# Kernel tuning notes

Hardware: AMD Instinct MI355X
Metric: run time of the kernel (lower is better)

## Reference

```python
import jax, jax.numpy as jnp
import numpy as np
from jax import lax

B, T_ENC, T_DEC, H, N_INP, OC = 1024, 48, 24, 128, 18, 0
F = N_INP - 1  # encoder1 input features (target column removed)


def _lstm_cell(x, h, c, Wih, Whh, bih, bhh):
    # PyTorch LSTMCell gate order: i, f, g, o
    g = x @ Wih.T + bih + h @ Whh.T + bhh
    i, f, gg, o = jnp.split(g, 4, axis=-1)
    c2 = jax.nn.sigmoid(f) * c + jax.nn.sigmoid(i) * jnp.tanh(gg)
    return jax.nn.sigmoid(o) * jnp.tanh(c2), c2


def setup_inputs() -> dict:
    key = jax.random.key(0)
    ks = jax.random.split(key, 32)
    w = lambda k, s: jax.random.normal(k, s, jnp.float32) * 0.05
    return {
        "input_p_q": jax.random.normal(ks[0], (B, T_ENC, N_INP), jnp.float32),
        "label_p": jax.random.normal(ks[1], (B, T_ENC), jnp.float32),
        "Ue1_W": w(ks[2], (T_ENC, T_ENC)), "Ue1_b": w(ks[3], (T_ENC,)),
        "We1_W": w(ks[4], (T_ENC, 2 * H)),
        "Ve1_W": w(ks[5], (1, T_ENC)), "Ve1_b": w(ks[6], (1,)),
        "Ue2_W": w(ks[7], (T_ENC, T_ENC)), "Ue2_b": w(ks[8], (T_ENC,)),
        "We2_W": w(ks[9], (T_ENC, 2 * H)),
        "Ve2_W": w(ks[10], (1, T_ENC)), "Ve2_b": w(ks[11], (1,)),
        "Ud_W": w(ks[12], (H, H)), "Ud_b": w(ks[13], (H,)),
        "Wd_W": w(ks[14], (H, 2 * H)),
        "Vd_W": w(ks[15], (1, H)), "Vd_b": w(ks[16], (1,)),
        "e1_Wih": w(ks[17], (4 * H, F)), "e1_Whh": w(ks[18], (4 * H, H)),
        "e1_bih": w(ks[19], (4 * H,)), "e1_bhh": w(ks[20], (4 * H,)),
        "e2_Wih": w(ks[21], (4 * H, H + 1)), "e2_Whh": w(ks[22], (4 * H, H)),
        "e2_bih": w(ks[23], (4 * H,)), "e2_bhh": w(ks[24], (4 * H,)),
        "d_Wih": w(ks[25], (4 * H, H)), "d_Whh": w(ks[26], (4 * H, H)),
        "d_bih": w(ks[27], (4 * H,)), "d_bhh": w(ks[28], (4 * H,)),
        "reg_W": w(ks[29], (1, H)), "reg_b": w(ks[30], (1,)),
    }


def reference(input_p_q, label_p, Ue1_W, Ue1_b, We1_W, Ve1_W, Ve1_b,
              Ue2_W, Ue2_b, We2_W, Ve2_W, Ve2_b, Ud_W, Ud_b, Wd_W, Vd_W, Vd_b,
              e1_Wih, e1_Whh, e1_bih, e1_bhh, e2_Wih, e2_Whh, e2_bih, e2_bhh,
              d_Wih, d_Whh, d_bih, d_bhh, reg_W, reg_b):
    b = input_p_q.shape[0]
    # drop the target column OC from the 18 input features
    x = jnp.concatenate([input_p_q[:, :T_ENC, :OC],
                         input_p_q[:, :T_ENC, OC + 1:N_INP]], axis=-1)  # [B,T,F]
    labels = label_p[:, :T_ENC]
    zeros = jnp.zeros((b, H), x.dtype)

    # ---- stage 1: spatial (input) attention + encoder1 LSTM ----
    pre1 = jnp.einsum('btf,st->bfs', x, Ue1_W) + Ue1_b  # Ue1(inputs^T), step-invariant: [B,F,T]

    def step1(carry, x_t):
        h, c = carry
        we = jnp.concatenate([h, c], axis=1) @ We1_W.T            # [B,T]
        e = jnp.tanh(we[:, None, :] + pre1)                        # [B,F,T]
        score = jnp.einsum('bft,t->bf', e, Ve1_W[0]) + Ve1_b[0]    # [B,F]
        h, c = _lstm_cell(x_t * jax.nn.softmax(score, axis=1), h, c,
                          e1_Wih, e1_Whh, e1_bih, e1_bhh)
        return (h, c), h

    _, mid = lax.scan(step1, (zeros, zeros), x.transpose(1, 0, 2))  # [T,B,H]
    mid = jnp.concatenate([mid.transpose(1, 0, 2), labels[:, :, None]], axis=2)  # [B,T,H+1]

    # ---- stage 2: second attention + encoder2 LSTM ----
    pre2 = jnp.einsum('btf,st->bfs', mid, Ue2_W) + Ue2_b  # [B,H+1,T]

    def step2(carry, m_t):
        h, c = carry
        we = jnp.concatenate([h, c], axis=1) @ We2_W.T            # [B,T]
        e = jnp.tanh(we[:, None, :] + pre2)                        # [B,H+1,T]
        score = jnp.einsum('bft,t->bf', e, Ve2_W[0]) + Ve2_b[0]    # [B,H+1]
        h, c = _lstm_cell(m_t * jax.nn.softmax(score, axis=1), h, c,
                          e2_Wih, e2_Whh, e2_bih, e2_bhh)
        return (h, c), h

    _, fin = lax.scan(step2, (zeros, zeros), mid.transpose(1, 0, 2))
    fin = fin.transpose(1, 0, 2)  # final_output: [B,T,H]

    # ---- decoder: temporal attention over final_output ----
    ud = fin @ Ud_W.T + Ud_b  # Ud(final_output), step-invariant: [B,T,H]

    def stepd(carry, _):
        hi, ci = carry
        wd = jnp.concatenate([hi, ci], axis=1) @ Wd_W.T            # [B,H]
        e = jnp.tanh(wd[:, None, :] + ud)                           # [B,T,H]
        score = jnp.einsum('bth,h->bt', e, Vd_W[0]) + Vd_b[0]       # [B,T]
        din = jnp.einsum('bt,bth->bh', jax.nn.softmax(score, axis=1), fin)
        hi, ci = _lstm_cell(din, hi, ci, d_Wih, d_Whh, d_bih, d_bhh)
        return (hi, ci), hi

    _, dec = lax.scan(stepd, (zeros, zeros), None, length=T_DEC + 6)  # [Td+6,B,H]
    out = dec.transpose(1, 0, 2) @ reg_W.T + reg_b                     # [B,Td+6,1]
    return out[:, -T_DEC:, 0]                                          # [B,T_DEC]
```

## Files before the change

### kernel.cpp

```cpp
#include <hip/hip_runtime.h>


#define T_ENC 48
#define H 128
#define FDIM 17
#define BBLK 2
#define NTH 512
#define GRID 512

#define H_WT1   0
#define H_WT2   77824
#define H_WTD   212992
#define H_WE1T  344064
#define H_WE2T  356352
#define H_WDT   368640
#define H_UDT   401408
#define F_B1    208896
#define F_B2    209408
#define F_BD    209920
#define F_MID   210432
#define F_FIN   6551040

typedef _Float16 h2_t __attribute__((ext_vector_type(2)));
union H2U { h2_t h; uint u; float f; };

__device__ __forceinline__ h2_t uh(uint v){ H2U x; x.u = v; return x.h; }
__device__ __forceinline__ h2_t fh(float v){ H2U x; x.f = v; return x.h; }
__device__ __forceinline__ uint pack2(float a, float b){
    H2U x; x.h[0] = (_Float16)a; x.h[1] = (_Float16)b; return x.u;
}
__device__ __forceinline__ float dot2f(h2_t a, h2_t b, float c){
#if __has_builtin(__builtin_amdgcn_fdot2)
    return __builtin_amdgcn_fdot2(a, b, c, false);
#else
    return c + (float)a[0]*(float)b[0] + (float)a[1]*(float)b[1];
#endif
}

__device__ __forceinline__ float fast_sigm(float x){
    return __fdividef(1.0f, 1.0f + __expf(-x));
}
__device__ __forceinline__ float fast_tanh(float x){
    float xc = fminf(fmaxf(x, -9.0f), 9.0f);
    float e = __expf(2.0f * xc);
    return __fdividef(e - 1.0f, e + 1.0f);
}

__global__ void prep_kernel(const float* __restrict__ We1W, const float* __restrict__ We2W,
                            const float* __restrict__ WdW,  const float* __restrict__ UdW,
                            const float* __restrict__ e1Wih, const float* __restrict__ e1Whh,
                            const float* __restrict__ e1bih, const float* __restrict__ e1bhh,
                            const float* __restrict__ e2Wih, const float* __restrict__ e2Whh,
                            const float* __restrict__ e2bih, const float* __restrict__ e2bhh,
                            const float* __restrict__ dWih,  const float* __restrict__ dWhh,
                            const float* __restrict__ dbih,  const float* __restrict__ dbhh,
                            float* __restrict__ ws)
{
    int idx = blockIdx.x * blockDim.x + threadIdx.x;
    _Float16* wsh = (_Float16*)ws;
    if (idx < 77824) {
        int k8 = idx >> 12, r = idx & 4095, j = r >> 3, kq = r & 7, k = k8*8 + kq;
        float v = 0.f;
        if (k < 17) v = e1Wih[j*17 + k]; else if (k < 145) v = e1Whh[j*128 + (k-17)];
        wsh[H_WT1 + idx] = (_Float16)v; return;
    }
    idx -= 77824;
    if (idx < 135168) {
        int k8 = idx >> 12, r = idx & 4095, j = r >> 3, kq = r & 7, k = k8*8 + kq;
        float v = 0.f;
        if (k < 129) v = e2Wih[j*129 + k]; else if (k < 257) v = e2Whh[j*128 + (k-129)];
        wsh[H_WT2 + idx] = (_Float16)v; return;
    }
    idx -= 135168;
    if (idx < 131072) {
        int k8 = idx >> 12, r = idx & 4095, j = r >> 3, kq = r & 7, k = k8*8 + kq;
        float v = (k < 128) ? dWih[j*128 + k] : dWhh[j*128 + (k-128)];
        wsh[H_WTD + idx] = (_Float16)v; return;
    }
    idx -= 131072;
    if (idx < 12288) {
        int pr = idx >> 1, p = idx & 1, k2 = pr / 48, s = pr % 48;
        wsh[H_WE1T + idx] = (_Float16)We1W[s*256 + 2*k2 + p]; return;
    }
    idx -= 12288;
    if (idx < 12288) {
        int pr = idx >> 1, p = idx & 1, k2 = pr / 48, s = pr % 48;
        wsh[H_WE2T + idx] = (_Float16)We2W[s*256 + 2*k2 + p]; return;
    }
    idx -= 12288;
    if (idx < 32768) {
        int pr = idx >> 1, p = idx & 1, k2 = pr >> 7, sp = pr & 127;
        wsh[H_WDT + idx] = (_Float16)WdW[sp*256 + 2*k2 + p]; return;
    }
    idx -= 32768;
    if (idx < 16384) {
        int pr = idx >> 1, p = idx & 1, k2 = pr >> 7, hh = pr & 127;
        wsh[H_UDT + idx] = (_Float16)UdW[hh*128 + 2*k2 + p]; return;
    }
    idx -= 16384;
    if (idx < 512) { ws[F_B1 + idx] = e1bih[idx] + e1bhh[idx]; return; }
    idx -= 512;
    if (idx < 512) { ws[F_B2 + idx] = e2bih[idx] + e2bhh[idx]; return; }
    idx -= 512;
    if (idx < 512) { ws[F_BD + idx] = dbih[idx] + dbhh[idx]; return; }
}

template<int K8>
__device__ __forceinline__ void lstm_gates2h(const float4* __restrict__ W8,
                                             const float* __restrict__ bias,
                                             const uint* u2, float* g, int tid)
{
    float a0 = bias[tid], a1 = a0;
    #pragma unroll 4
    for (int k8 = 0; k8 < K8; ++k8) {
        float4 w  = W8[k8*512 + tid];
        float4 ua = *(const float4*)(u2 + 4*k8);
        float4 ub = *(const float4*)(u2 + 132 + 4*k8);
        a0 = dot2f(fh(w.x), fh(ua.x), a0); a0 = dot2f(fh(w.y), fh(ua.y), a0);
        a0 = dot2f(fh(w.z), fh(ua.z), a0); a0 = dot2f(fh(w.w), fh(ua.w), a0);
        a1 = dot2f(fh(w.x), fh(ub.x), a1); a1 = dot2f(fh(w.y), fh(ub.y), a1);
        a1 = dot2f(fh(w.z), fh(ub.z), a1); a1 = dot2f(fh(w.w), fh(ub.w), a1);
    }
    g[tid] = a0; g[512 + tid] = a1;
}

__device__ __forceinline__ void softmax2(float* sc, float* at, int n, int tid)
{
    if (tid < 64) {
        int b = tid >> 5, i = tid & 31, base = b*129;
        float m = -1e30f;
        for (int f = i; f < n; f += 32) m = fmaxf(m, sc[base + f]);
        for (int o = 16; o; o >>= 1) m = fmaxf(m, __shfl_xor(m, o, 32));
        float ssum = 0.f;
        for (int f = i; f < n; f += 32) { float p = __expf(sc[base+f] - m); at[base+f] = p; ssum += p; }
        for (int o = 16; o; o >>= 1) ssum += __shfl_xor(ssum, o, 32);
        float inv = __fdividef(1.f, ssum);
        for (int f = i; f < n; f += 32) at[base + f] *= inv;
    }
}

__device__ __forceinline__ void we_phase_h(const uint* __restrict__ W2,
                                           const uint* h2, const uint* c2,
                                           float* sh_we, int tid)
{
    if (tid < 384) {
        int b = tid / 192, r = tid % 192, s = r >> 2, kq = r & 3;
        const uint* st2 = ((kq < 2) ? h2 : c2) + b*64 + (kq & 1)*32;
        const uint* w2  = W2 + (kq*32)*48 + s;
        float acc = 0.f;
        #pragma unroll 8
        for (int kk = 0; kk < 32; ++kk)
            acc = dot2f(uh(st2[kk]), uh(w2[kk*48]), acc);
        acc += __shfl_xor(acc, 1);
        acc += __shfl_xor(acc, 2);
        if (kq == 0) sh_we[b*48 + s] = acc;
    }
}

__global__ __launch_bounds__(NTH, 6)
void dstp_main(const float* __restrict__ ipq,  const float* __restrict__ labp,
               const float* __restrict__ Ue1W, const float* __restrict__ Ue1b,
               const float* __restrict__ Ve1,  const float* __restrict__ Ve1b,
               const float* __restrict__ Ue2W, const float* __restrict__ Ue2b,
               const float* __restrict__ Ve2,  const float* __restrict__ Ve2b,
               const float* __restrict__ Udb,
               const float* __restrict__ Vd,   const float* __restrict__ Vdb,
               const float* __restrict__ regW, const float* __restrict__ regb,
               float* __restrict__ ws, float* __restrict__ out)
{
    extern __shared__ float sm[];
    float* sh_h   = sm;
    float* sh_c   = sm + 256;
    float* sh_we  = sm + 512;
    float* sh_sc  = sm + 768;
    float* sh_at  = sm + 1028;
    float* sh_g   = sm + 1288;
    float* sh_x   = sm + 2312;
    float* sh_p1  = sm + 3944;
    uint*  sh_h2u = (uint*)(sm + 5576);
    uint*  sh_c2u = (uint*)(sm + 5704);
    uint*  sh_u2  = (uint*)(sm + 5832);
    _Float16* sh_bigh = (_Float16*)(sm + 6096);

    const int tid = threadIdx.x;
    const int b0  = blockIdx.x * BBLK;
    const _Float16* wsh = (const _Float16*)ws;

    for (int idx = tid; idx < BBLK*T_ENC*FDIM; idx += NTH) {
        int b = idx / (T_ENC*FDIM), r = idx % (T_ENC*FDIM), t = r / FDIM, f = r % FDIM;
        sh_x[idx] = ipq[((size_t)(b0 + b)*T_ENC + t)*18 + 1 + f];
    }
    if (tid < 256) { sh_h[tid] = 0.f; sh_c[tid] = 0.f; }
    if (tid < 128) { sh_h2u[tid] = 0u; sh_c2u[tid] = 0u; }
    if (tid < BBLK*T_ENC) {
        int b = tid / T_ENC, t = tid % T_ENC;
        ws[F_MID + ((size_t)(b0 + b)*T_ENC + t)*129 + 128] = labp[(size_t)(b0 + b)*T_ENC + t];
    }
    __syncthreads();
    for (int idx = tid; idx < BBLK*T_ENC*FDIM; idx += NTH) {
        int b = idx / (T_ENC*FDIM), r = idx % (T_ENC*FDIM), s = r / FDIM, f = r % FDIM;
        float acc = Ue1b[s];
        #pragma unroll 4
        for (int t = 0; t < T_ENC; ++t) acc = fmaf(sh_x[(b*T_ENC+t)*FDIM + f], Ue1W[s*T_ENC + t], acc);
        sh_p1[(b*T_ENC + s)*FDIM + f] = acc;
    }
    __syncthreads();

    const float ve1b = Ve1b[0];
    for (int t = 0; t < T_ENC; ++t) {
        we_phase_h((const uint*)(wsh + H_WE1T), sh_h2u, sh_c2u, sh_we, tid);
        __syncthreads();
        if (tid < 136) {
            int pair = tid >> 2, q = tid & 3, b = pair / FDIM, f = pair % FDIM;
            float acc = 0.f;
            for (int s = q; s < 48; s += 4)
                acc += fast_tanh(sh_we[b*48 + s] + sh_p1[(b*T_ENC + s)*FDIM + f]) * Ve1[s];
            acc += __shfl_xor(acc, 1);
            acc += __shfl_xor(acc, 2);
            if (q == 0) sh_sc[b*129 + f] = acc + ve1b;
        }
        __syncthreads();
        softmax2(sh_sc, sh_at, FDIM, tid);
        __syncthreads();
        if (tid < BBLK*152) {
            int b = tid / 152, kk = tid % 152;
            float v;
            if (kk < FDIM)        v = sh_x[(b*T_ENC + t)*FDIM + kk] * sh_at[b*129 + kk];
            else if (kk < FDIM+H) v = sh_h[b*H + (kk - FDIM)];
            else                  v = 0.f;
            float vnb = __shfl_xor(v, 1);
            if (!(tid & 1)) sh_u2[b*132 + (kk >> 1)] = pack2(v, vnb);
        }
        __syncthreads();
        lstm_gates2h<19>((const float4*)(wsh + H_WT1), ws + F_B1, sh_u2, sh_g, tid);
        __syncthreads();
        if (tid < 256) {
            int b = tid >> 7, jj = tid & 127;
            float gi = sh_g[b*512 + jj],       gf = sh_g[b*512 + 128 + jj];
            float gg = sh_g[b*512 + 256 + jj], go = sh_g[b*512 + 384 + jj];
            float c2v = fast_sigm(gf)*sh_c[tid] + fast_sigm(gi)*fast_tanh(gg);
            float hn  = fast_sigm(go)*fast_tanh(c2v);
            sh_c[tid] = c2v; sh_h[tid] = hn;
            ws[F_MID + ((size_t)(b0 + b)*T_ENC + t)*129 + jj] = hn;
            float hnb = __shfl_xor(hn, 1), cnb = __shfl_xor(c2v, 1);
            if (!(jj & 1)) {
                sh_h2u[b*64 + (jj >> 1)] = pack2(hn, hnb);
                sh_c2u[b*64 + (jj >> 1)] = pack2(c2v, cnb);
            }
        }
        __syncthreads();
    }

    for (int idx = tid; idx < BBLK*48*129; idx += NTH) {
        int b = idx / (48*129), r = idx % (48*129), s = r / 129, f = r % 129;
        const float* midb = ws + F_MID + (size_t)(b0 + b)*T_ENC*129 + f;
        float acc = Ue2b[s];
        #pragma unroll 4
        for (int t2 = 0; t2 < T_ENC; ++t2) acc = fmaf(midb[t2*129], Ue2W[s*48 + t2], acc);
        sh_bigh[(b*48 + s)*130 + f] = (_Float16)acc;
    }
    if (tid < 256) { sh_h[tid] = 0.f; sh_c[tid] = 0.f; }
    if (tid < 128) { sh_h2u[tid] = 0u; sh_c2u[tid] = 0u; }
    __syncthreads();

    const float ve2b = Ve2b[0];
    for (int t = 0; t < T_ENC; ++t) {
        we_phase_h((const uint*)(wsh + H_WE2T), sh_h2u, sh_c2u, sh_we, tid);
        __syncthreads();
        if (tid < 258) {
            int b = tid / 129, f = tid % 129;
            const _Float16* p2 = sh_bigh + b*48*130 + f;
            const float* wv = sh_we + b*48;
            float acc = 0.f;
            #pragma unroll 4
            for (int s = 0; s < 48; ++s)
                acc += fast_tanh(wv[s] + (float)p2[s*130]) * Ve2[s];
            sh_sc[b*129 + f] = acc + ve2b;
        }
        __syncthreads();
        softmax2(sh_sc, sh_at, 129, tid);
        __syncthreads();
        for (int idx = tid; idx < BBLK*264; idx += NTH) {
            int b = idx / 264, kk = idx % 264;
            const float* midrow = ws + F_MID + ((size_t)(b0 + b)*T_ENC + t)*129;
            float v;
            if (kk < 129)      v = midrow[kk] * sh_at[b*129 + kk];
            else if (kk < 257) v = sh_h[b*H + (kk - 129)];
            else               v = 0.f;
            float vnb = __shfl_xor(v, 1);
            if (!(idx & 1)) sh_u2[b*132 + ((kk) >> 1)] = pack2(v, vnb);
        }
        __syncthreads();
        lstm_gates2h<33>((const float4*)(wsh + H_WT2), ws + F_B2, sh_u2, sh_g, tid);
        __syncthreads();
        if (tid < 256) {
            int b = tid >> 7, jj = tid & 127;
            float gi = sh_g[b*512 + jj],       gf = sh_g[b*512 + 128 + jj];
            float gg = sh_g[b*512 + 256 + jj], go = sh_g[b*512 + 384 + jj];
            float c2v = fast_sigm(gf)*sh_c[tid] + fast_sigm(gi)*fast_tanh(gg);
            float hn  = fast_sigm(go)*fast_tanh(c2v);
            sh_c[tid] = c2v; sh_h[tid] = hn;
            ws[F_FIN + ((size_t)(b0 + b)*T_ENC + t)*128 + jj] = hn;
            float hnb = __shfl_xor(hn, 1), cnb = __shfl_xor(c2v, 1);
            if (!(jj & 1)) {
                sh_h2u[b*64 + (jj >> 1)] = pack2(hn, hnb);
                sh_c2u[b*64 + (jj >> 1)] = pack2(c2v, cnb);
            }
        }
        __syncthreads();
    }

    {
        uint* fin2 = (uint*)sh_bigh;
        const float4* fsrc = (const float4*)(ws + F_FIN + (size_t)b0*T_ENC*128);
        for (int idx = tid; idx < BBLK*T_ENC*32; idx += NTH) {
            float4 v = fsrc[idx];
            fin2[2*idx]     = pack2(v.x, v.y);
            fin2[2*idx + 1] = pack2(v.z, v.w);
        }
    }
    __syncthreads();
    {
        const int hh = tid & 127;
        const uint* UT2  = (const uint*)(wsh + H_UDT);
        const uint* fin2 = (const uint*)sh_bigh;
        float* uds = ws + F_MID + (size_t)b0*T_ENC*129;
        #pragma unroll
        for (int c = 0; c < 3; ++c) {
            float acc[8]; int rowb2[8];
            #pragma unroll
            for (int i = 0; i < 8; ++i) {
                int idx = (c*8 + i)*NTH + tid;
                int b = idx / 6144, r = idx % 6144, tt = r >> 7;
                rowb2[i] = (b*T_ENC + tt)*64;
                acc[i] = Udb[hh];
            }
            for (int k2 = 0; k2 < 64; ++k2) {
                h2_t w2 = uh(UT2[k2*128 + hh]);
                #pragma unroll
                for (int i = 0; i < 8; ++i) acc[i] = dot2f(uh(fin2[rowb2[i] + k2]), w2, acc[i]);
            }
            #pragma unroll
            for (int i = 0; i < 8; ++i) uds[(size_t)(c*8 + i)*NTH + tid] = acc[i];
        }
    }
    if (tid < 256) { sh_h[tid] = 0.f; sh_c[tid] = 0.f; }
    if (tid < 128) { sh_h2u[tid] = 0u; sh_c2u[tid] = 0u; }
    __syncthreads();
    {
        const float* uds = ws + F_MID + (size_t)b0*T_ENC*129;
        for (int idx = tid; idx < BBLK*T_ENC*128; idx += NTH) {
            int b = idx / 6144, r = idx % 6144, tt = r >> 7, h2i = r & 127;
            sh_bigh[(b*T_ENC + tt)*130 + h2i] = (_Float16)uds[idx];
        }
    }
    __syncthreads();

    const float vdb = Vdb[0], rb = regb[0];
    const float* fing = ws + F_FIN + (size_t)b0*T_ENC*128;
    for (int st = 0; st < 30; ++st) {
        {
            int b = tid >> 8, r = tid & 255, kh = r >> 7, sp = r & 127;
            const uint* st2 = (kh ? sh_c2u : sh_h2u) + b*64;
            const uint* W2  = (const uint*)(wsh + H_WDT) + (kh*64)*128 + sp;
            float acc = 0.f;
            #pragma unroll 8
            for (int kk = 0; kk < 64; ++kk)
                acc = dot2f(uh(st2[kk]), uh(W2[kk*128]), acc);
            sh_g[(b*2 + kh)*128 + sp] = acc;
        }
        __syncthreads();
        if (tid < 192) {
            int q = tid & 1, pair = tid >> 1, b = pair / 48, tt = pair % 48;
            const float* pg = sh_g + b*256;
            const _Float16* udrow = sh_bigh + (b*T_ENC + tt)*130;
            float acc = 0.f;
            int h0 = q*64;
            #pragma unroll 4
            for (int kk = 0; kk < 64; ++kk) {
                int hh = h0 + kk;
                float wd = pg[hh] + pg[128 + hh];
                acc += fast_tanh(wd + (float)udrow[hh]) * Vd[hh];
            }
            acc += __shfl_xor(acc, 1);
            if (q == 0) sh_sc[b*129 + tt] = acc + vdb;
        }
        __syncthreads();
        softmax2(sh_sc, sh_at, 48, tid);
        __syncthreads();
        if (tid < 256) {
            int b = tid >> 7, hh = tid & 127;
            const float* fb = fing + b*T_ENC*128 + hh;
            float acc = 0.f;
            #pragma unroll 4
            for (int tt = 0; tt < 48; ++tt) acc = fmaf(sh_at[b*129 + tt], fb[tt*128], acc);
            float anb = __shfl_xor(acc, 1);
            if (!(hh & 1)) sh_u2[b*132 + (hh >> 1)] = pack2(acc, anb);
        }
        if (tid < 128) {
            int b = tid >> 6, i = tid & 63;
            sh_u2[b*132 + 64 + i] = sh_h2u[b*64 + i];
        }
        __syncthreads();
        lstm_gates2h<32>((const float4*)(wsh + H_WTD), ws + F_BD, sh_u2, sh_g, tid);
        __syncthreads();
        if (tid < 256) {
            int b = tid >> 7, jj = tid & 127;
            float gi = sh_g[b*512 + jj],       gf = sh_g[b*512 + 128 + jj];
            float gg = sh_g[b*512 + 256 + jj], go = sh_g[b*512 + 384 + jj];
            float c2v = fast_sigm(gf)*sh_c[tid] + fast_sigm(gi)*fast_tanh(gg);
            float hn  = fast_sigm(go)*fast_tanh(c2v);
            sh_c[tid] = c2v; sh_h[tid] = hn;
            float hnb = __shfl_xor(hn, 1), cnb = __shfl_xor(c2v, 1);
            if (!(jj & 1)) {
                sh_h2u[b*64 + (jj >> 1)] = pack2(hn, hnb);
                sh_c2u[b*64 + (jj >> 1)] = pack2(c2v, cnb);
            }
        }
        __syncthreads();
        if (st >= 6 && tid < 128) {
            int b = tid >> 6, l = tid & 63;
            float v = sh_h[b*H + l]*regW[l] + sh_h[b*H + 64 + l]*regW[64 + l];
            for (int o = 32; o; o >>= 1) v += __shfl_xor(v, o);
            if (l == 0) out[(size_t)(b0 + b)*24 + (st - 6)] = v + rb;
        }
    }
}

extern "C" void kernel_launch(void* const* d_in, const int* in_sizes, int n_in,
                              void* d_out, int out_size, void* d_ws, size_t ws_size,
                              hipStream_t stream)
{
    const float* ipq   = (const float*)d_in[0];
    const float* labp  = (const float*)d_in[1];
    const float* Ue1W  = (const float*)d_in[2];
    const float* Ue1b  = (const float*)d_in[3];
    const float* We1W  = (const float*)d_in[4];
    const float* Ve1   = (const float*)d_in[5];
    const float* Ve1b  = (const float*)d_in[6];
    const float* Ue2W  = (const float*)d_in[7];
    const float* Ue2b  = (const float*)d_in[8];
    const float* We2W  = (const float*)d_in[9];
    const float* Ve2   = (const float*)d_in[10];
    const float* Ve2b  = (const float*)d_in[11];
    const float* UdW   = (const float*)d_in[12];
    const float* Udb   = (const float*)d_in[13];
    const float* WdW   = (const float*)d_in[14];
    const float* Vd    = (const float*)d_in[15];
    const float* Vdb   = (const float*)d_in[16];
    const float* e1Wih = (const float*)d_in[17];
    const float* e1Whh = (const float*)d_in[18];
    const float* e1bih = (const float*)d_in[19];
    const float* e1bhh = (const float*)d_in[20];
    const float* e2Wih = (const float*)d_in[21];
    const float* e2Whh = (const float*)d_in[22];
    const float* e2bih = (const float*)d_in[23];
    const float* e2bhh = (const float*)d_in[24];
    const float* dWih  = (const float*)d_in[25];
    const float* dWhh  = (const float*)d_in[26];
    const float* dbih  = (const float*)d_in[27];
    const float* dbhh  = (const float*)d_in[28];
    const float* regW  = (const float*)d_in[29];
    const float* regb  = (const float*)d_in[30];
    float* ws  = (float*)d_ws;
    float* out = (float*)d_out;

    prep_kernel<<<(417792 + 1536 + 255)/256, 256, 0, stream>>>(
        We1W, We2W, WdW, UdW,
        e1Wih, e1Whh, e1bih, e1bhh,
        e2Wih, e2Whh, e2bih, e2bhh,
        dWih, dWhh, dbih, dbhh, ws);

    const size_t smem = 12336u * sizeof(float);
    hipFuncSetAttribute((const void*)dstp_main,
                        hipFuncAttributeMaxDynamicSharedMemorySize, (int)smem);
    dstp_main<<<GRID, NTH, smem, stream>>>(
        ipq, labp, Ue1W, Ue1b, Ve1, Ve1b,
        Ue2W, Ue2b, Ve2, Ve2b,
        Udb, Vd, Vdb, regW, regb, ws, out);
}
```

Measured before the change: 1.814 ms.

## Double block threads, split per-step reductions, keep final_output in LDS as fp16

```diff
diff --git a/kernel.cpp b/kernel.cpp
--- a/kernel.cpp
+++ b/kernel.cpp
@@ -5,7 +5,7 @@
 #define H 128
 #define FDIM 17
 #define BBLK 2
-#define NTH 512
+#define NTH 1024
 #define GRID 512
 
 #define H_WT1   0
@@ -19,7 +19,6 @@
 #define F_B2    209408
 #define F_BD    209920
 #define F_MID   210432
-#define F_FIN   6551040
 
 typedef _Float16 h2_t __attribute__((ext_vector_type(2)));
 union H2U { h2_t h; uint u; float f; };
@@ -106,28 +105,38 @@
 }
 
 template<int K8>
-__device__ __forceinline__ void lstm_gates2h(const float4* __restrict__ W8,
+__device__ __forceinline__ void lstm_gates2w(const float4* __restrict__ W8,
                                              const float* __restrict__ bias,
-                                             const uint* u2, float* g, int tid)
-{
-    float a0 = bias[tid], a1 = a0;
-    #pragma unroll 4
-    for (int k8 = 0; k8 < K8; ++k8) {
-        float4 w  = W8[k8*512 + tid];
-        float4 ua = *(const float4*)(u2 + 4*k8);
-        float4 ub = *(const float4*)(u2 + 132 + 4*k8);
-        a0 = dot2f(fh(w.x), fh(ua.x), a0); a0 = dot2f(fh(w.y), fh(ua.y), a0);
-        a0 = dot2f(fh(w.z), fh(ua.z), a0); a0 = dot2f(fh(w.w), fh(ua.w), a0);
-        a1 = dot2f(fh(w.x), fh(ub.x), a1); a1 = dot2f(fh(w.y), fh(ub.y), a1);
-        a1 = dot2f(fh(w.z), fh(ub.z), a1); a1 = dot2f(fh(w.w), fh(ub.w), a1);
-    }
-    g[tid] = a0; g[512 + tid] = a1;
+                                             const uint* __restrict__ u2all,
+                                             float* __restrict__ g, int tid)
+{
+    const int b = tid >> 9, j = tid & 511;
+    const uint* u2 = u2all + b*132;
+    float a0 = bias[j], a1 = 0.f;
+    #pragma unroll
+    for (int k8 = 0; k8 + 1 < K8; k8 += 2) {
+        float4 w0 = W8[k8*512 + j];
+        float4 w1 = W8[(k8+1)*512 + j];
+        float4 u0 = *(const float4*)(u2 + 4*k8);
+        float4 u1 = *(const float4*)(u2 + 4*k8 + 4);
+        a0 = dot2f(fh(w0.x), fh(u0.x), a0); a0 = dot2f(fh(w0.y), fh(u0.y), a0);
+        a0 = dot2f(fh(w0.z), fh(u0.z), a0); a0 = dot2f(fh(w0.w), fh(u0.w), a0);
+        a1 = dot2f(fh(w1.x), fh(u1.x), a1); a1 = dot2f(fh(w1.y), fh(u1.y), a1);
+        a1 = dot2f(fh(w1.z), fh(u1.z), a1); a1 = dot2f(fh(w1.w), fh(u1.w), a1);
+    }
+    if (K8 & 1) {
+        float4 w0 = W8[(K8-1)*512 + j];
+        float4 u0 = *(const float4*)(u2 + 4*(K8-1));
+        a0 = dot2f(fh(w0.x), fh(u0.x), a0); a0 = dot2f(fh(w0.y), fh(u0.y), a0);
+        a0 = dot2f(fh(w0.z), fh(u0.z), a0); a0 = dot2f(fh(w0.w), fh(u0.w), a0);
+    }
+    g[b*512 + j] = a0 + a1;
 }
 
 __device__ __forceinline__ void softmax2(float* sc, float* at, int n, int tid)
 {
     if (tid < 64) {
-        int b = tid >> 5, i = tid & 31, base = b*129;
+        int b = tid >> 5, i = tid & 31, base = b*132;
         float m = -1e30f;
         for (int f = i; f < n; f += 32) m = fmaxf(m, sc[base + f]);
         for (int o = 16; o; o >>= 1) m = fmaxf(m, __shfl_xor(m, o, 32));
@@ -139,25 +148,26 @@
     }
 }
 
-__device__ __forceinline__ void we_phase_h(const uint* __restrict__ W2,
+__device__ __forceinline__ void we_phase2w(const uint* __restrict__ W2,
                                            const uint* h2, const uint* c2,
                                            float* sh_we, int tid)
 {
-    if (tid < 384) {
-        int b = tid / 192, r = tid % 192, s = r >> 2, kq = r & 3;
-        const uint* st2 = ((kq < 2) ? h2 : c2) + b*64 + (kq & 1)*32;
-        const uint* w2  = W2 + (kq*32)*48 + s;
+    if (tid < 768) {
+        int b = tid / 384, r = tid % 384, s = r >> 3, kq = r & 7;
+        const uint* st2 = ((kq < 4) ? h2 : c2) + b*64 + (kq & 3)*16;
+        const uint* w2  = W2 + (kq*16)*48 + s;
         float acc = 0.f;
-        #pragma unroll 8
-        for (int kk = 0; kk < 32; ++kk)
-            acc = dot2f(uh(st2[kk]), uh(w2[kk*48]), acc);
+        #pragma unroll
+        for (int i = 0; i < 16; ++i)
+            acc = dot2f(uh(st2[i]), uh(w2[i*48]), acc);
         acc += __shfl_xor(acc, 1);
         acc += __shfl_xor(acc, 2);
+        acc += __shfl_xor(acc, 4);
         if (kq == 0) sh_we[b*48 + s] = acc;
     }
 }
 
-__global__ __launch_bounds__(NTH, 6)
+__global__ __launch_bounds__(NTH, 8)
 void dstp_main(const float* __restrict__ ipq,  const float* __restrict__ labp,
                const float* __restrict__ Ue1W, const float* __restrict__ Ue1b,
                const float* __restrict__ Ve1,  const float* __restrict__ Ve1b,
@@ -172,15 +182,18 @@
     float* sh_h   = sm;
     float* sh_c   = sm + 256;
     float* sh_we  = sm + 512;
-    float* sh_sc  = sm + 768;
-    float* sh_at  = sm + 1028;
-    float* sh_g   = sm + 1288;
-    float* sh_x   = sm + 2312;
-    float* sh_p1  = sm + 3944;
-    uint*  sh_h2u = (uint*)(sm + 5576);
-    uint*  sh_c2u = (uint*)(sm + 5704);
-    uint*  sh_u2  = (uint*)(sm + 5832);
-    _Float16* sh_bigh = (_Float16*)(sm + 6096);
+    float* sh_sc  = sm + 608;
+    float* sh_sc2 = sm + 872;
+    float* sh_at  = sm + 1136;
+    float* sh_g   = sm + 1400;
+    float* sh_x   = sm + 2424;
+    float* sh_p1  = sm + 4056;
+    uint*  sh_h2u = (uint*)(sm + 5688);
+    uint*  sh_c2u = (uint*)(sm + 5816);
+    uint*  sh_u2  = (uint*)(sm + 5944);
+    _Float16* sh_p2h = (_Float16*)(sm + 6212);
+    _Float16* sh_fnh = (_Float16*)(sm + 12452);
+    uint*     sh_fn2 = (uint*)(sm + 12452);
 
     const int tid = threadIdx.x;
     const int b0  = blockIdx.x * BBLK;
@@ -202,22 +215,23 @@
         float acc = Ue1b[s];
         #pragma unroll 4
         for (int t = 0; t < T_ENC; ++t) acc = fmaf(sh_x[(b*T_ENC+t)*FDIM + f], Ue1W[s*T_ENC + t], acc);
-        sh_p1[(b*T_ENC + s)*FDIM + f] = acc;
+        sh_p1[idx] = acc;
     }
     __syncthreads();
 
     const float ve1b = Ve1b[0];
     for (int t = 0; t < T_ENC; ++t) {
-        we_phase_h((const uint*)(wsh + H_WE1T), sh_h2u, sh_c2u, sh_we, tid);
-        __syncthreads();
-        if (tid < 136) {
-            int pair = tid >> 2, q = tid & 3, b = pair / FDIM, f = pair % FDIM;
+        we_phase2w((const uint*)(wsh + H_WE1T), sh_h2u, sh_c2u, sh_we, tid);
+        __syncthreads();
+        if (tid < 272) {
+            int b = tid / 136, r = tid % 136, f = r >> 3, q = r & 7;
             float acc = 0.f;
-            for (int s = q; s < 48; s += 4)
+            for (int s = q; s < 48; s += 8)
                 acc += fast_tanh(sh_we[b*48 + s] + sh_p1[(b*T_ENC + s)*FDIM + f]) * Ve1[s];
             acc += __shfl_xor(acc, 1);
             acc += __shfl_xor(acc, 2);
-            if (q == 0) sh_sc[b*129 + f] = acc + ve1b;
+            acc += __shfl_xor(acc, 4);
+            if (q == 0) sh_sc[b*132 + f] = acc + ve1b;
         }
         __syncthreads();
         softmax2(sh_sc, sh_at, FDIM, tid);
@@ -225,14 +239,14 @@
         if (tid < BBLK*152) {
             int b = tid / 152, kk = tid % 152;
             float v;
-            if (kk < FDIM)        v = sh_x[(b*T_ENC + t)*FDIM + kk] * sh_at[b*129 + kk];
+            if (kk < FDIM)        v = sh_x[(b*T_ENC + t)*FDIM + kk] * sh_at[b*132 + kk];
             else if (kk < FDIM+H) v = sh_h[b*H + (kk - FDIM)];
             else                  v = 0.f;
             float vnb = __shfl_xor(v, 1);
-            if (!(tid & 1)) sh_u2[b*132 + (kk >> 1)] = pack2(v, vnb);
-        }
-        __syncthreads();
-        lstm_gates2h<19>((const float4*)(wsh + H_WT1), ws + F_B1, sh_u2, sh_g, tid);
+            if (!(kk & 1)) sh_u2[b*132 + (kk >> 1)] = pack2(v, vnb);
+        }
+        __syncthreads();
+        lstm_gates2w<19>((const float4*)(wsh + H_WT1), ws + F_B1, sh_u2, sh_g, tid);
         __syncthreads();
         if (tid < 256) {
             int b = tid >> 7, jj = tid & 127;
@@ -257,7 +271,7 @@
         float acc = Ue2b[s];
         #pragma unroll 4
         for (int t2 = 0; t2 < T_ENC; ++t2) acc = fmaf(midb[t2*129], Ue2W[s*48 + t2], acc);
-        sh_bigh[(b*48 + s)*130 + f] = (_Float16)acc;
+        sh_p2h[(b*48 + s)*130 + f] = (_Float16)acc;
     }
     if (tid < 256) { sh_h[tid] = 0.f; sh_c[tid] = 0.f; }
     if (tid < 128) { sh_h2u[tid] = 0u; sh_c2u[tid] = 0u; }
@@ -265,33 +279,40 @@
 
     const float ve2b = Ve2b[0];
     for (int t = 0; t < T_ENC; ++t) {
-        we_phase_h((const uint*)(wsh + H_WE2T), sh_h2u, sh_c2u, sh_we, tid);
-        __syncthreads();
-        if (tid < 258) {
-            int b = tid / 129, f = tid % 129;
-            const _Float16* p2 = sh_bigh + b*48*130 + f;
+        we_phase2w((const uint*)(wsh + H_WE2T), sh_h2u, sh_c2u, sh_we, tid);
+        __syncthreads();
+        if (tid < 516) {
+            int b = tid / 258, r = tid % 258;
+            int f  = (r < 129) ? r : r - 129;
+            int s0 = (r < 129) ? 0 : 24;
+            const _Float16* p2 = sh_p2h + (b*48)*130 + f;
             const float* wv = sh_we + b*48;
             float acc = 0.f;
             #pragma unroll 4
-            for (int s = 0; s < 48; ++s)
+            for (int s = s0; s < s0 + 24; ++s)
                 acc += fast_tanh(wv[s] + (float)p2[s*130]) * Ve2[s];
-            sh_sc[b*129 + f] = acc + ve2b;
+            ((r < 129) ? sh_sc : sh_sc2)[b*132 + f] = acc;
+        }
+        __syncthreads();
+        if (tid < 258) {
+            int b = tid / 129, f = tid % 129;
+            sh_sc[b*132 + f] += sh_sc2[b*132 + f] + ve2b;
         }
         __syncthreads();
         softmax2(sh_sc, sh_at, 129, tid);
         __syncthreads();
-        for (int idx = tid; idx < BBLK*264; idx += NTH) {
-            int b = idx / 264, kk = idx % 264;
+        if (tid < BBLK*264) {
+            int b = tid / 264, kk = tid % 264;
             const float* midrow = ws + F_MID + ((size_t)(b0 + b)*T_ENC + t)*129;
             float v;
-            if (kk < 129)      v = midrow[kk] * sh_at[b*129 + kk];
+            if (kk < 129)      v = midrow[kk] * sh_at[b*132 + kk];
             else if (kk < 257) v = sh_h[b*H + (kk - 129)];
             else               v = 0.f;
             float vnb = __shfl_xor(v, 1);
-            if (!(idx & 1)) sh_u2[b*132 + ((kk) >> 1)] = pack2(v, vnb);
-        }
-        __syncthreads();
-        lstm_gates2h<33>((const float4*)(wsh + H_WT2), ws + F_B2, sh_u2, sh_g, tid);
+            if (!(kk & 1)) sh_u2[b*132 + (kk >> 1)] = pack2(v, vnb);
+        }
+        __syncthreads();
+        lstm_gates2w<33>((const float4*)(wsh + H_WT2), ws + F_B2, sh_u2, sh_g, tid);
         __syncthreads();
         if (tid < 256) {
             int b = tid >> 7, jj = tid & 127;
@@ -300,7 +321,7 @@
             float c2v = fast_sigm(gf)*sh_c[tid] + fast_sigm(gi)*fast_tanh(gg);
             float hn  = fast_sigm(go)*fast_tanh(c2v);
             sh_c[tid] = c2v; sh_h[tid] = hn;
-            ws[F_FIN + ((size_t)(b0 + b)*T_ENC + t)*128 + jj] = hn;
+            sh_fnh[(b*T_ENC + t)*128 + jj] = (_Float16)hn;
             float hnb = __shfl_xor(hn, 1), cnb = __shfl_xor(c2v, 1);
             if (!(jj & 1)) {
                 sh_h2u[b*64 + (jj >> 1)] = pack2(hn, hnb);
@@ -311,98 +332,76 @@
     }
 
     {
-        uint* fin2 = (uint*)sh_bigh;
-        const float4* fsrc = (const float4*)(ws + F_FIN + (size_t)b0*T_ENC*128);
-        for (int idx = tid; idx < BBLK*T_ENC*32; idx += NTH) {
-            float4 v = fsrc[idx];
-            fin2[2*idx]     = pack2(v.x, v.y);
-            fin2[2*idx + 1] = pack2(v.z, v.w);
-        }
-    }
-    __syncthreads();
-    {
-        const int hh = tid & 127;
+        int b = tid >> 9, r = tid & 511, hh = r & 127, tg = r >> 7;
+        float acc[12];
+        float ub = Udb[hh];
+        #pragma unroll
+        for (int i = 0; i < 12; ++i) acc[i] = ub;
         const uint* UT2  = (const uint*)(wsh + H_UDT);
-        const uint* fin2 = (const uint*)sh_bigh;
-        float* uds = ws + F_MID + (size_t)b0*T_ENC*129;
+        const uint* fin2 = sh_fn2 + b*T_ENC*64;
+        for (int k2 = 0; k2 < 64; ++k2) {
+            h2_t w2 = uh(UT2[k2*128 + hh]);
+            #pragma unroll
+            for (int i = 0; i < 12; ++i)
+                acc[i] = dot2f(uh(fin2[(tg + 4*i)*64 + k2]), w2, acc[i]);
+        }
         #pragma unroll
-        for (int c = 0; c < 3; ++c) {
-            float acc[8]; int rowb2[8];
-            #pragma unroll
-            for (int i = 0; i < 8; ++i) {
-                int idx = (c*8 + i)*NTH + tid;
-                int b = idx / 6144, r = idx % 6144, tt = r >> 7;
-                rowb2[i] = (b*T_ENC + tt)*64;
-                acc[i] = Udb[hh];
-            }
-            for (int k2 = 0; k2 < 64; ++k2) {
-                h2_t w2 = uh(UT2[k2*128 + hh]);
-                #pragma unroll
-                for (int i = 0; i < 8; ++i) acc[i] = dot2f(uh(fin2[rowb2[i] + k2]), w2, acc[i]);
-            }
-            #pragma unroll
-            for (int i = 0; i < 8; ++i) uds[(size_t)(c*8 + i)*NTH + tid] = acc[i];
-        }
+        for (int i = 0; i < 12; ++i)
+            sh_p2h[(b*T_ENC + tg + 4*i)*130 + hh] = (_Float16)acc[i];
     }
     if (tid < 256) { sh_h[tid] = 0.f; sh_c[tid] = 0.f; }
     if (tid < 128) { sh_h2u[tid] = 0u; sh_c2u[tid] = 0u; }
     __syncthreads();
-    {
-        const float* uds = ws + F_MID + (size_t)b0*T_ENC*129;
-        for (int idx = tid; idx < BBLK*T_ENC*128; idx += NTH) {
-            int b = idx / 6144, r = idx % 6144, tt = r >> 7, h2i = r & 127;
-            sh_bigh[(b*T_ENC + tt)*130 + h2i] = (_Float16)uds[idx];
-        }
-    }
-    __syncthreads();
 
     const float vdb = Vdb[0], rb = regb[0];
-    const float* fing = ws + F_FIN + (size_t)b0*T_ENC*128;
     for (int st = 0; st < 30; ++st) {
         {
-            int b = tid >> 8, r = tid & 255, kh = r >> 7, sp = r & 127;
-            const uint* st2 = (kh ? sh_c2u : sh_h2u) + b*64;
-            const uint* W2  = (const uint*)(wsh + H_WDT) + (kh*64)*128 + sp;
+            int b = tid >> 9, r = tid & 511, kq = r >> 7, sp = r & 127;
+            const uint* st2 = ((kq < 2) ? sh_h2u : sh_c2u) + b*64 + (kq & 1)*32;
+            const uint* W2  = (const uint*)(wsh + H_WDT) + (kq*32)*128 + sp;
             float acc = 0.f;
             #pragma unroll 8
-            for (int kk = 0; kk < 64; ++kk)
-                acc = dot2f(uh(st2[kk]), uh(W2[kk*128]), acc);
-            sh_g[(b*2 + kh)*128 + sp] = acc;
-        }
-        __syncthreads();
-        if (tid < 192) {
-            int q = tid & 1, pair = tid >> 1, b = pair / 48, tt = pair % 48;
-            const float* pg = sh_g + b*256;
-            const _Float16* udrow = sh_bigh + (b*T_ENC + tt)*130;
+            for (int i = 0; i < 32; ++i)
+                acc = dot2f(uh(st2[i]), uh(W2[i*128]), acc);
+            sh_g[b*512 + kq*128 + sp] = acc;
+        }
+        __syncthreads();
+        if (tid < 768) {
+            int b = tid / 384, r = tid % 384, tt = r >> 3, q = r & 7, h0 = q*16;
+            const _Float16* udrow = sh_p2h + (b*T_ENC + tt)*130;
+            const float* pg = sh_g + b*512;
             float acc = 0.f;
-            int h0 = q*64;
             #pragma unroll 4
-            for (int kk = 0; kk < 64; ++kk) {
+            for (int kk = 0; kk < 16; ++kk) {
                 int hh = h0 + kk;
-                float wd = pg[hh] + pg[128 + hh];
+                float wd = pg[hh] + pg[128 + hh] + pg[256 + hh] + pg[384 + hh];
                 acc += fast_tanh(wd + (float)udrow[hh]) * Vd[hh];
             }
             acc += __shfl_xor(acc, 1);
-            if (q == 0) sh_sc[b*129 + tt] = acc + vdb;
+            acc += __shfl_xor(acc, 2);
+            acc += __shfl_xor(acc, 4);
+            if (q == 0) sh_sc[b*132 + tt] = acc + vdb;
         }
         __syncthreads();
         softmax2(sh_sc, sh_at, 48, tid);
         __syncthreads();
-        if (tid < 256) {
-            int b = tid >> 7, hh = tid & 127;
-            const float* fb = fing + b*T_ENC*128 + hh;
+        {
+            int b = tid >> 9, r = tid & 511, hh = r >> 2, q = r & 3;
+            const _Float16* fb = sh_fnh + b*T_ENC*128 + hh;
             float acc = 0.f;
-            #pragma unroll 4
-            for (int tt = 0; tt < 48; ++tt) acc = fmaf(sh_at[b*129 + tt], fb[tt*128], acc);
-            float anb = __shfl_xor(acc, 1);
-            if (!(hh & 1)) sh_u2[b*132 + (hh >> 1)] = pack2(acc, anb);
+            for (int tt = q; tt < 48; tt += 4)
+                acc = fmaf(sh_at[b*132 + tt], (float)fb[tt*128], acc);
+            acc += __shfl_xor(acc, 1);
+            acc += __shfl_xor(acc, 2);
+            float anb = __shfl_xor(acc, 4);
+            if (q == 0 && !(hh & 1)) sh_u2[b*132 + (hh >> 1)] = pack2(acc, anb);
         }
         if (tid < 128) {
             int b = tid >> 6, i = tid & 63;
             sh_u2[b*132 + 64 + i] = sh_h2u[b*64 + i];
         }
         __syncthreads();
-        lstm_gates2h<32>((const float4*)(wsh + H_WTD), ws + F_BD, sh_u2, sh_g, tid);
+        lstm_gates2w<32>((const float4*)(wsh + H_WTD), ws + F_BD, sh_u2, sh_g, tid);
         __syncthreads();
         if (tid < 256) {
             int b = tid >> 7, jj = tid & 127;
@@ -471,7 +470,7 @@
         e2Wih, e2Whh, e2bih, e2bhh,
         dWih, dWhh, dbih, dbhh, ws);
 
-    const size_t smem = 12336u * sizeof(float);
+    const size_t smem = 18596u * sizeof(float);
     hipFuncSetAttribute((const void*)dstp_main,
                         hipFuncAttributeMaxDynamicSharedMemorySize, (int)smem);
     dstp_main<<<GRID, NTH, smem, stream>>>(
```

Measured after the change: 3.141 ms. +73.2%, slower.

## Keep encoder2 outputs and Ud projection in LDS, widen attention score parallelism

Applied to the files above, without the earlier changes.

```diff
diff --git a/kernel.cpp b/kernel.cpp
--- a/kernel.cpp
+++ b/kernel.cpp
@@ -19,7 +19,6 @@
 #define F_B2    209408
 #define F_BD    209920
 #define F_MID   210432
-#define F_FIN   6551040
 
 typedef _Float16 h2_t __attribute__((ext_vector_type(2)));
 union H2U { h2_t h; uint u; float f; };
@@ -38,12 +37,11 @@
 }
 
 __device__ __forceinline__ float fast_sigm(float x){
-    return __fdividef(1.0f, 1.0f + __expf(-x));
+    return __builtin_amdgcn_rcpf(1.0f + __expf(-x));
 }
 __device__ __forceinline__ float fast_tanh(float x){
-    float xc = fminf(fmaxf(x, -9.0f), 9.0f);
-    float e = __expf(2.0f * xc);
-    return __fdividef(e - 1.0f, e + 1.0f);
+    float e = __expf(2.0f * x);
+    return fmaf(-2.0f, __builtin_amdgcn_rcpf(1.0f + e), 1.0f);
 }
 
 __global__ void prep_kernel(const float* __restrict__ We1W, const float* __restrict__ We2W,
@@ -127,7 +125,7 @@
 __device__ __forceinline__ void softmax2(float* sc, float* at, int n, int tid)
 {
     if (tid < 64) {
-        int b = tid >> 5, i = tid & 31, base = b*129;
+        int b = tid >> 5, i = tid & 31, base = b*132;
         float m = -1e30f;
         for (int f = i; f < n; f += 32) m = fmaxf(m, sc[base + f]);
         for (int o = 16; o; o >>= 1) m = fmaxf(m, __shfl_xor(m, o, 32));
@@ -172,15 +170,18 @@
     float* sh_h   = sm;
     float* sh_c   = sm + 256;
     float* sh_we  = sm + 512;
-    float* sh_sc  = sm + 768;
-    float* sh_at  = sm + 1028;
-    float* sh_g   = sm + 1288;
-    float* sh_x   = sm + 2312;
-    float* sh_p1  = sm + 3944;
-    uint*  sh_h2u = (uint*)(sm + 5576);
-    uint*  sh_c2u = (uint*)(sm + 5704);
-    uint*  sh_u2  = (uint*)(sm + 5832);
-    _Float16* sh_bigh = (_Float16*)(sm + 6096);
+    float* sh_sc  = sm + 608;
+    float* sh_sc2 = sm + 872;
+    float* sh_at  = sm + 1136;
+    float* sh_g   = sm + 1400;
+    float* sh_x   = sm + 2424;
+    float* sh_p1  = sm + 4056;
+    uint*  sh_h2u = (uint*)(sm + 5688);
+    uint*  sh_c2u = (uint*)(sm + 5816);
+    uint*  sh_u2  = (uint*)(sm + 5944);
+    _Float16* sh_p2h = (_Float16*)(sm + 6212);
+    _Float16* sh_fnh = (_Float16*)(sm + 12452);
+    uint*     sh_fn2 = (uint*)(sm + 12452);
 
     const int tid = threadIdx.x;
     const int b0  = blockIdx.x * BBLK;
@@ -202,7 +203,7 @@
         float acc = Ue1b[s];
         #pragma unroll 4
         for (int t = 0; t < T_ENC; ++t) acc = fmaf(sh_x[(b*T_ENC+t)*FDIM + f], Ue1W[s*T_ENC + t], acc);
-        sh_p1[(b*T_ENC + s)*FDIM + f] = acc;
+        sh_p1[idx] = acc;
     }
     __syncthreads();
 
@@ -210,14 +211,15 @@
     for (int t = 0; t < T_ENC; ++t) {
         we_phase_h((const uint*)(wsh + H_WE1T), sh_h2u, sh_c2u, sh_we, tid);
         __syncthreads();
-        if (tid < 136) {
-            int pair = tid >> 2, q = tid & 3, b = pair / FDIM, f = pair % FDIM;
+        if (tid < 272) {
+            int b = tid / 136, r = tid % 136, f = r >> 3, q = r & 7;
             float acc = 0.f;
-            for (int s = q; s < 48; s += 4)
+            for (int s = q; s < 48; s += 8)
                 acc += fast_tanh(sh_we[b*48 + s] + sh_p1[(b*T_ENC + s)*FDIM + f]) * Ve1[s];
             acc += __shfl_xor(acc, 1);
             acc += __shfl_xor(acc, 2);
-            if (q == 0) sh_sc[b*129 + f] = acc + ve1b;
+            acc += __shfl_xor(acc, 4);
+            if (q == 0) sh_sc[b*132 + f] = acc + ve1b;
         }
         __syncthreads();
         softmax2(sh_sc, sh_at, FDIM, tid);
@@ -225,11 +227,11 @@
         if (tid < BBLK*152) {
             int b = tid / 152, kk = tid % 152;
             float v;
-            if (kk < FDIM)        v = sh_x[(b*T_ENC + t)*FDIM + kk] * sh_at[b*129 + kk];
+            if (kk < FDIM)        v = sh_x[(b*T_ENC + t)*FDIM + kk] * sh_at[b*132 + kk];
             else if (kk < FDIM+H) v = sh_h[b*H + (kk - FDIM)];
             else                  v = 0.f;
             float vnb = __shfl_xor(v, 1);
-            if (!(tid & 1)) sh_u2[b*132 + (kk >> 1)] = pack2(v, vnb);
+            if (!(kk & 1)) sh_u2[b*132 + (kk >> 1)] = pack2(v, vnb);
         }
         __syncthreads();
         lstm_gates2h<19>((const float4*)(wsh + H_WT1), ws + F_B1, sh_u2, sh_g, tid);
@@ -257,7 +259,7 @@
         float acc = Ue2b[s];
         #pragma unroll 4
         for (int t2 = 0; t2 < T_ENC; ++t2) acc = fmaf(midb[t2*129], Ue2W[s*48 + t2], acc);
-        sh_bigh[(b*48 + s)*130 + f] = (_Float16)acc;
+        sh_p2h[(b*48 + s)*130 + f] = (_Float16)acc;
     }
     if (tid < 256) { sh_h[tid] = 0.f; sh_c[tid] = 0.f; }
     if (tid < 128) { sh_h2u[tid] = 0u; sh_c2u[tid] = 0u; }
@@ -267,15 +269,22 @@
     for (int t = 0; t < T_ENC; ++t) {
         we_phase_h((const uint*)(wsh + H_WE2T), sh_h2u, sh_c2u, sh_we, tid);
         __syncthreads();
-        if (tid < 258) {
-            int b = tid / 129, f = tid % 129;
-            const _Float16* p2 = sh_bigh + b*48*130 + f;
+        for (int p = tid; p < 516; p += NTH) {
+            int b = p / 258, r = p % 258;
+            int f  = (r < 129) ? r : r - 129;
+            int s0 = (r < 129) ? 0 : 24;
+            const _Float16* p2 = sh_p2h + (b*48)*130 + f;
             const float* wv = sh_we + b*48;
             float acc = 0.f;
             #pragma unroll 4
-            for (int s = 0; s < 48; ++s)
+            for (int s = s0; s < s0 + 24; ++s)
                 acc += fast_tanh(wv[s] + (float)p2[s*130]) * Ve2[s];
-            sh_sc[b*129 + f] = acc + ve2b;
+            ((r < 129) ? sh_sc : sh_sc2)[b*132 + f] = acc;
+        }
+        __syncthreads();
+        if (tid < 258) {
+            int b = tid / 129, f = tid % 129;
+            sh_sc[b*132 + f] += sh_sc2[b*132 + f] + ve2b;
         }
         __syncthreads();
         softmax2(sh_sc, sh_at, 129, tid);
@@ -284,11 +293,11 @@
             int b = idx / 264, kk = idx % 264;
             const float* midrow = ws + F_MID + ((size_t)(b0 + b)*T_ENC + t)*129;
             float v;
-            if (kk < 129)      v = midrow[kk] * sh_at[b*129 + kk];
+            if (kk < 129)      v = midrow[kk] * sh_at[b*132 + kk];
             else if (kk < 257) v = sh_h[b*H + (kk - 129)];
             else               v = 0.f;
             float vnb = __shfl_xor(v, 1);
-            if (!(idx & 1)) sh_u2[b*132 + ((kk) >> 1)] = pack2(v, vnb);
+            if (!(idx & 1)) sh_u2[b*132 + (kk >> 1)] = pack2(v, vnb);
         }
         __syncthreads();
         lstm_gates2h<33>((const float4*)(wsh + H_WT2), ws + F_B2, sh_u2, sh_g, tid);
@@ -300,7 +309,7 @@
             float c2v = fast_sigm(gf)*sh_c[tid] + fast_sigm(gi)*fast_tanh(gg);
             float hn  = fast_sigm(go)*fast_tanh(c2v);
             sh_c[tid] = c2v; sh_h[tid] = hn;
-            ws[F_FIN + ((size_t)(b0 + b)*T_ENC + t)*128 + jj] = hn;
+            sh_fnh[(b*T_ENC + t)*128 + jj] = (_Float16)hn;
             float hnb = __shfl_xor(hn, 1), cnb = __shfl_xor(c2v, 1);
             if (!(jj & 1)) {
                 sh_h2u[b*64 + (jj >> 1)] = pack2(hn, hnb);
@@ -311,53 +320,33 @@
     }
 
     {
-        uint* fin2 = (uint*)sh_bigh;
-        const float4* fsrc = (const float4*)(ws + F_FIN + (size_t)b0*T_ENC*128);
-        for (int idx = tid; idx < BBLK*T_ENC*32; idx += NTH) {
-            float4 v = fsrc[idx];
-            fin2[2*idx]     = pack2(v.x, v.y);
-            fin2[2*idx + 1] = pack2(v.z, v.w);
-        }
-    }
-    __syncthreads();
-    {
         const int hh = tid & 127;
-        const uint* UT2  = (const uint*)(wsh + H_UDT);
-        const uint* fin2 = (const uint*)sh_bigh;
-        float* uds = ws + F_MID + (size_t)b0*T_ENC*129;
+        const uint* UT2 = (const uint*)(wsh + H_UDT);
         #pragma unroll
         for (int c = 0; c < 3; ++c) {
-            float acc[8]; int rowb2[8];
+            float acc[8]; int rowb2[8]; int rowp[8];
             #pragma unroll
             for (int i = 0; i < 8; ++i) {
                 int idx = (c*8 + i)*NTH + tid;
                 int b = idx / 6144, r = idx % 6144, tt = r >> 7;
                 rowb2[i] = (b*T_ENC + tt)*64;
+                rowp[i]  = (b*T_ENC + tt)*130 + hh;
                 acc[i] = Udb[hh];
             }
             for (int k2 = 0; k2 < 64; ++k2) {
                 h2_t w2 = uh(UT2[k2*128 + hh]);
                 #pragma unroll
-                for (int i = 0; i < 8; ++i) acc[i] = dot2f(uh(fin2[rowb2[i] + k2]), w2, acc[i]);
+                for (int i = 0; i < 8; ++i) acc[i] = dot2f(uh(sh_fn2[rowb2[i] + k2]), w2, acc[i]);
             }
             #pragma unroll
-            for (int i = 0; i < 8; ++i) uds[(size_t)(c*8 + i)*NTH + tid] = acc[i];
+            for (int i = 0; i < 8; ++i) sh_p2h[rowp[i]] = (_Float16)acc[i];
         }
     }
     if (tid < 256) { sh_h[tid] = 0.f; sh_c[tid] = 0.f; }
     if (tid < 128) { sh_h2u[tid] = 0u; sh_c2u[tid] = 0u; }
     __syncthreads();
-    {
-        const float* uds = ws + F_MID + (size_t)b0*T_ENC*129;
-        for (int idx = tid; idx < BBLK*T_ENC*128; idx += NTH) {
-            int b = idx / 6144, r = idx % 6144, tt = r >> 7, h2i = r & 127;
-            sh_bigh[(b*T_ENC + tt)*130 + h2i] = (_Float16)uds[idx];
-        }
-    }
-    __syncthreads();
 
     const float vdb = Vdb[0], rb = regb[0];
-    const float* fing = ws + F_FIN + (size_t)b0*T_ENC*128;
     for (int st = 0; st < 30; ++st) {
         {
             int b = tid >> 8, r = tid & 255, kh = r >> 7, sp = r & 127;
@@ -370,32 +359,33 @@
             sh_g[(b*2 + kh)*128 + sp] = acc;
         }
         __syncthreads();
-        if (tid < 192) {
-            int q = tid & 1, pair = tid >> 1, b = pair / 48, tt = pair % 48;
+        if (tid < 384) {
+            int b = tid / 192, r = tid % 192, tt = r >> 2, q = r & 3, h0 = q*32;
+            const _Float16* udrow = sh_p2h + (b*T_ENC + tt)*130;
             const float* pg = sh_g + b*256;
-            const _Float16* udrow = sh_bigh + (b*T_ENC + tt)*130;
             float acc = 0.f;
-            int h0 = q*64;
             #pragma unroll 4
-            for (int kk = 0; kk < 64; ++kk) {
+            for (int kk = 0; kk < 32; ++kk) {
                 int hh = h0 + kk;
                 float wd = pg[hh] + pg[128 + hh];
                 acc += fast_tanh(wd + (float)udrow[hh]) * Vd[hh];
             }
             acc += __shfl_xor(acc, 1);
-            if (q == 0) sh_sc[b*129 + tt] = acc + vdb;
+            acc += __shfl_xor(acc, 2);
+            if (q == 0) sh_sc[b*132 + tt] = acc + vdb;
         }
         __syncthreads();
         softmax2(sh_sc, sh_at, 48, tid);
         __syncthreads();
-        if (tid < 256) {
-            int b = tid >> 7, hh = tid & 127;
-            const float* fb = fing + b*T_ENC*128 + hh;
+        {
+            int b = tid >> 8, r = tid & 255, hh = r >> 1, q = r & 1;
+            const _Float16* fb = sh_fnh + b*T_ENC*128 + hh;
             float acc = 0.f;
-            #pragma unroll 4
-            for (int tt = 0; tt < 48; ++tt) acc = fmaf(sh_at[b*129 + tt], fb[tt*128], acc);
-            float anb = __shfl_xor(acc, 1);
-            if (!(hh & 1)) sh_u2[b*132 + (hh >> 1)] = pack2(acc, anb);
+            for (int tt = q; tt < 48; tt += 2)
+                acc = fmaf(sh_at[b*132 + tt], (float)fb[tt*128], acc);
+            acc += __shfl_xor(acc, 1);
+            float anb = __shfl_xor(acc, 2);
+            if (!(tid & 3)) sh_u2[b*132 + (hh >> 1)] = pack2(acc, anb);
         }
         if (tid < 128) {
             int b = tid >> 6, i = tid & 63;
@@ -471,7 +461,7 @@
         e2Wih, e2Whh, e2bih, e2bhh,
         dWih, dWhh, dbih, dbhh, ws);
 
-    const size_t smem = 12336u * sizeof(float);
+    const size_t smem = 18596u * sizeof(float);
     hipFuncSetAttribute((const void*)dstp_main,
                         hipFuncAttributeMaxDynamicSharedMemorySize, (int)smem);
     dstp_main<<<GRID, NTH, smem, stream>>>(
```

Measured after the change: 1.485 ms. 18.1% less time.
